# Kernel tuning notes

Measured on AMD Instinct MI355X. Metric: run time of the kernel, lower is better.

## Reference

```python
import jax, jax.numpy as jnp
import numpy as np
import math

HEADS = 16
SPH = 64      # size_per_head
KEY = 64      # key_size (defaults to size_per_head)
EMB = 1024
STEP = 3


def extract_seq_patches(x, kernel_size, step):
    # x: [B, L, D] -> [B, L, kernel_size, D]; patch j at pos t is x_pad[t - p_left + j*step]
    B, L, D = x.shape
    k_size = kernel_size + (step - 1) * (kernel_size - 1)
    p_right = (k_size - 1) // 2
    p_left = k_size - 1 - p_right
    xp = jnp.pad(x, ((0, 0), (p_left, p_right), (0, 0)))
    xs = [xp[:, i:i + L] for i in range(0, k_size, step)]  # kernel_size slices
    return jnp.stack(xs, axis=2)


def setup_inputs() -> dict:
    key = jax.random.key(0)
    kx, kq, kk, kv = jax.random.split(key, 4)
    B, L = 2, 4096
    x = jax.random.normal(kx, (B, L, EMB), dtype=jnp.float32)
    W_q = jax.random.normal(kq, (EMB, HEADS * KEY), dtype=jnp.float32) * 0.02
    W_k = jax.random.normal(kk, (EMB, HEADS * KEY), dtype=jnp.float32) * 0.02
    W_v = jax.random.normal(kv, (EMB, HEADS * SPH), dtype=jnp.float32) * 0.02
    return {"x": x, "W_q": W_q, "W_k": W_k, "W_v": W_v}


def _forward(x, W_q, W_k, W_v):
    B, L, D = x.shape
    pad_len = STEP - L % STEP
    x = jnp.pad(x, ((0, 0), (0, pad_len), (0, 0)))
    new_len = L + pad_len
    blocks = new_len // STEP
    q = x @ W_q  # [B, new_len, H*KEY]
    k = x @ W_k
    v = x @ W_v
    ksz = 1 + 2 * (STEP - 1)  # kernel_size = 5
    kp = extract_seq_patches(k, ksz, STEP)  # [B, new_len, ksz, H*KEY]
    vp = extract_seq_patches(v, ksz, STEP)
    # reshape to [B, H, step, blocks, d]
    q = q.reshape(B, blocks, STEP, HEADS, KEY).transpose(0, 3, 2, 1, 4)
    kb = k.reshape(B, blocks, STEP, HEADS, KEY).transpose(0, 3, 2, 1, 4)
    vb = v.reshape(B, blocks, STEP, HEADS, SPH).transpose(0, 3, 2, 1, 4)
    # neighbor patches: [B, H, step, blocks, ksz, d]
    kp = kp.reshape(B, blocks, STEP, ksz, HEADS, KEY).transpose(0, 4, 2, 1, 3, 5)
    vp = vp.reshape(B, blocks, STEP, ksz, HEADS, SPH).transpose(0, 4, 2, 1, 3, 5)
    scale = 1.0 / math.sqrt(KEY)
    # strided attention over blocks (same residue mod step): [B,H,step,blocks,blocks]
    a = jnp.einsum('bhsqk,bhspk->bhsqp', q, kb) * scale
    # block-local neighbor attention: [B,H,step,blocks,ksz]
    ap = jnp.einsum('bhsqk,bhsqnk->bhsqn', q, kp) * scale
    A = jax.nn.softmax(jnp.concatenate([a, ap], axis=-1), axis=-1)
    a, ap = A[..., :blocks], A[..., blocks:]
    o = (jnp.einsum('bhsqp,bhspd->bhsqd', a, vb)
         + jnp.einsum('bhsqn,bhsqnd->bhsqd', ap, vp))
    o = o.transpose(0, 3, 2, 1, 4).reshape(B, new_len, HEADS * SPH)
    return o[:, :L]


def reference(x, W_q, W_k, W_v):
    return _forward(x, W_q, W_k, W_v)
```

## Files before the change

### kernel.cpp

```cpp
#include <hip/hip_runtime.h>
#include <hip/hip_bf16.h>

typedef unsigned int u32;
typedef unsigned short u16;
typedef short s8v __attribute__((ext_vector_type(8)));
typedef short s4v __attribute__((ext_vector_type(4)));
typedef float f4v __attribute__((ext_vector_type(4)));
typedef float f16v __attribute__((ext_vector_type(16)));
typedef u32 u32x2 __attribute__((ext_vector_type(2)));

#define NBLK 1366
#define VROW 1376
#define QSCALE 0.18033688011112042f

__device__ __forceinline__ u16 f2b(float f) {
  u32 u = __builtin_bit_cast(u32, f);
  u = (u + 0x7FFFu + ((u >> 16) & 1u)) >> 16;
  return (u16)u;
}

__device__ __forceinline__ u32 cvtpk(float a, float b) {
  u32 r;
  asm("v_cvt_pk_bf16_f32 %0, %1, %2" : "=v"(r) : "v"(a), "v"(b));
  return r;
}

__device__ __forceinline__ float fexp2(float x) {
#if defined(__has_builtin)
#if __has_builtin(__builtin_amdgcn_exp2f)
  return __builtin_amdgcn_exp2f(x);
#define FEXP2_DONE 1
#endif
#endif
#ifndef FEXP2_DONE
  float r;
  asm("v_exp_f32 %0, %1" : "=v"(r) : "v"(x));
  return r;
#endif
}

__device__ __forceinline__ void gll16(const void* g, void* l) {
  __builtin_amdgcn_global_load_lds(
      (const __attribute__((address_space(1))) u32*)g,
      (__attribute__((address_space(3))) u32*)l, 16, 0, 0);
}

__device__ __forceinline__ f4v mfma32(s8v a, s8v b, f4v c) {
  return __builtin_amdgcn_mfma_f32_16x16x32_bf16(a, b, c, 0, 0, 0);
}

__device__ __forceinline__ f16v mfma3216(s8v a, s8v b, f16v c) {
  return __builtin_amdgcn_mfma_f32_32x32x16_bf16(a, b, c, 0, 0, 0);
}

__device__ __forceinline__ f16v mfma3208(s4v a, s4v b, f16v c) {
#if defined(__has_builtin)
#if __has_builtin(__builtin_amdgcn_mfma_f32_32x32x8bf16_1k)
#define MFMA3208_BUILTIN 1
#endif
#endif
#ifdef MFMA3208_BUILTIN
  return __builtin_amdgcn_mfma_f32_32x32x8bf16_1k(a, b, c, 0, 0, 0);
#else
  f16v d;
  asm("v_mfma_f32_32x32x8_bf16 %0, %1, %2, %3" : "=v"(d) : "v"(a), "v"(b), "v"(c));
  return d;
#endif
}

__global__ __launch_bounds__(256) void k_prep(const float* __restrict__ x,
                                              const float* __restrict__ Wq,
                                              const float* __restrict__ Wk,
                                              const float* __restrict__ Wv,
                                              u16* __restrict__ xb,
                                              u16* __restrict__ Wt,
                                              u16* __restrict__ Vt) {
  const int bid = blockIdx.x;
  const int tid = threadIdx.x;
  if (bid < 4160) {
    long base = ((long)bid * 256 + tid) * 8;
    if (base >= 8320L * 1024L) return;
    int m = (int)(base >> 10);
    int c = (int)(base & 1023);
    int b = m / 4098;
    int t = m - b * 4098;
    s8v pack;
    if (m < 8196 && t < 4096) {
      const float* src = x + ((size_t)b * 4096 + t) * 1024 + c;
      float4 v0 = *(const float4*)(src);
      float4 v1 = *(const float4*)(src + 4);
      pack[0] = (short)f2b(v0.x); pack[1] = (short)f2b(v0.y);
      pack[2] = (short)f2b(v0.z); pack[3] = (short)f2b(v0.w);
      pack[4] = (short)f2b(v1.x); pack[5] = (short)f2b(v1.y);
      pack[6] = (short)f2b(v1.z); pack[7] = (short)f2b(v1.w);
    } else {
#pragma unroll
      for (int i = 0; i < 8; ++i) pack[i] = 0;
    }
    *(s8v*)(xb + base) = pack;
  } else if (bid < 7232) {
    __shared__ float tile[32][33];
    int bid3 = bid - 4160;
    int z = bid3 >> 10;
    int rem = bid3 & 1023;
    const float* W = (z == 0) ? Wq : ((z == 1) ? Wk : Wv);
    u16* dst = Wt + (size_t)z * 1024 * 1024;
    int n0 = (rem & 31) * 32, k0 = (rem >> 5) * 32;
    int tx = tid & 31, ty = tid >> 5;
#pragma unroll
    for (int i = 0; i < 4; ++i)
      tile[ty + i * 8][tx] = W[(size_t)(k0 + ty + i * 8) * 1024 + n0 + tx];
    __syncthreads();
#pragma unroll
    for (int i = 0; i < 4; ++i)
      dst[(size_t)(n0 + ty + i * 8) * 1024 + k0 + tx] = f2b(tile[tx][ty + i * 8]);
  } else {
    int gidx = (bid - 7232) * 256 + tid;
    if (gidx < 6144) {
      u16* dst = Vt + (size_t)gidx * VROW + NBLK;
#pragma unroll
      for (int i = 0; i < 10; ++i) dst[i] = 0;
    } else if (gidx < 6400) {
      Vt[(size_t)6144 * VROW + (gidx - 6144)] = 0;
    }
  }
}

__global__ __launch_bounds__(256) void k_gemm_qkv(const u16* __restrict__ xb,
                                                  const u16* __restrict__ Wt,
                                                  u16* __restrict__ Qp,
                                                  u16* __restrict__ Kp,
                                                  u16* __restrict__ Vt) {
  const int zid = blockIdx.z;
  const int m0 = blockIdx.x * 128;
  const int n0 = blockIdx.y * 128;
  const u16* Bg = Wt + (size_t)zid * 1024 * 1024 + (size_t)n0 * 1024;

  __shared__ __align__(16) u16 shl[16384];
  u16* A0 = shl;
  u16* A1 = shl + 4096;
  u16* B0 = shl + 8192;
  u16* B1 = shl + 12288;

  const int tid = threadIdx.x;
  const int lane = tid & 63;
  const int w = tid >> 6;
  const int wr = w >> 1, wc = w & 1;
  const int lo = lane & 15, g = lane >> 4;

  const int lrow = lane >> 2;
  const int csrc = (lane & 3) ^ ((lane >> 3) & 3);
  const int rsw = (g ^ ((lo >> 1) & 3)) << 4;

  f4v acc[4][4];
#pragma unroll
  for (int i = 0; i < 4; ++i)
#pragma unroll
    for (int j = 0; j < 4; ++j) {
      f4v z = {0.f, 0.f, 0.f, 0.f};
      acc[i][j] = z;
    }

  auto stage = [&](int kt, u16* Ab, u16* Bb) {
#pragma unroll
    for (int c = 0; c < 2; ++c) {
      int rloc = w * 32 + c * 16 + lrow;
      gll16(xb + (size_t)(m0 + rloc) * 1024 + kt + csrc * 8,
            Ab + (w * 32 + c * 16) * 32);
      gll16(Bg + (size_t)rloc * 1024 + kt + csrc * 8,
            Bb + (w * 32 + c * 16) * 32);
    }
  };

  auto compute = [&](const u16* Ab, const u16* Bb) {
    s8v af[4], bf[4];
#pragma unroll
    for (int i = 0; i < 4; ++i) {
      int ar = wr * 64 + i * 16 + lo;
      af[i] = *(const s8v*)((const char*)Ab + ar * 64 + rsw);
      int br = wc * 64 + i * 16 + lo;
      bf[i] = *(const s8v*)((const char*)Bb + br * 64 + rsw);
    }
    __builtin_amdgcn_s_setprio(1);
#pragma unroll
    for (int i = 0; i < 4; ++i)
#pragma unroll
      for (int j = 0; j < 4; ++j)
        acc[i][j] = mfma32(af[i], bf[j], acc[i][j]);
    __builtin_amdgcn_s_setprio(0);
  };

#define BAR_VM4                                             \
  asm volatile("s_waitcnt vmcnt(4)" ::: "memory");          \
  __builtin_amdgcn_s_barrier();                             \
  asm volatile("" ::: "memory");
#define BAR_LGKM                                            \
  asm volatile("s_waitcnt lgkmcnt(0)" ::: "memory");        \
  __builtin_amdgcn_s_barrier();                             \
  asm volatile("" ::: "memory");

  stage(0, A0, B0);
#pragma unroll 1
  for (int kk = 0; kk < 15; ++kk) {
    int kt = kk * 64;
    stage(kt + 32, A1, B1);
    BAR_VM4
    compute(A0, B0);
    BAR_LGKM
    stage(kt + 64, A0, B0);
    BAR_VM4
    compute(A1, B1);
    BAR_LGKM
  }
  stage(31 * 32, A1, B1);
  BAR_VM4
  compute(A0, B0);
  BAR_LGKM
  asm volatile("s_waitcnt vmcnt(0)" ::: "memory");
  __builtin_amdgcn_s_barrier();
  asm volatile("" ::: "memory");
  compute(A1, B1);
  __syncthreads();

#undef BAR_VM4
#undef BAR_LGKM

  const float esc = (zid == 0) ? QSCALE : 1.0f;
  if (zid != 2) {
    u16* dq = (zid == 0) ? Qp : Kp;
#pragma unroll
    for (int i = 0; i < 4; ++i) {
#pragma unroll
      for (int r = 0; r < 4; ++r) {
        int m = m0 + wr * 64 + i * 16 + g * 4 + r;
        if (m >= 8196) continue;
        int b = m / 4098;
        int t = m - b * 4098;
        int s = t % 3;
        int p = t / 3;
        int cb = (b * 3 + s) * 16;
#pragma unroll
        for (int j = 0; j < 4; ++j) {
          int n = n0 + wc * 64 + j * 16 + lo;
          int h = n >> 6, d = n & 63;
          dq[(size_t)((cb + h) * NBLK + p) * 64 + d] = f2b(acc[i][j][r] * esc);
        }
      }
    }
  } else {
    u16* tile = shl;
#pragma unroll
    for (int i = 0; i < 4; ++i)
#pragma unroll
      for (int r = 0; r < 4; ++r) {
        int ml = wr * 64 + i * 16 + g * 4 + r;
#pragma unroll
        for (int j = 0; j < 4; ++j) {
          int nl = wc * 64 + j * 16 + lo;
          tile[ml * 128 + nl] = f2b(acc[i][j][r]);
        }
      }
    __syncthreads();
    for (int pair = tid; pair < 384; pair += 256) {
      int nl = pair & 127;
      int s = pair >> 7;
      int n = n0 + nl;
      int h = n >> 6, d = n & 63;
      for (int b = 0; b < 2; ++b) {
        int mlo = m0 > b * 4098 ? m0 : b * 4098;
        int cap = b * 4098 + 4096;
        int mhi = (m0 + 128 < cap) ? m0 + 128 : cap;
        if (mlo >= mhi) continue;
        int t_lo = mlo - b * 4098;
        int add = (s - (t_lo % 3) + 3) % 3;
        int t = t_lo + add;
        int tend = mhi - b * 4098;
        u16* dst = Vt + (size_t)(((b * 3 + s) * 16 + h) * 64 + d) * VROW;
        for (; t < tend; t += 3)
          dst[t / 3] = tile[(b * 4098 + t - m0) * 128 + nl];
      }
    }
  }
}

__global__ __launch_bounds__(256, 4) void k_attn(const u16* __restrict__ Qp,
                                                 const u16* __restrict__ Kp,
                                                 const u16* __restrict__ Vt,
                                                 float* __restrict__ out) {
  const int wg = blockIdx.x;
  const int idx = (wg & 7) * 132 + (wg >> 3);
  const int combo = idx / 11;
  const int qb = idx - combo * 11;
  const int b = combo / 48;
  const int rem = combo - b * 48;
  const int s = rem >> 4;
  const int h = rem & 15;
  const int tid = threadIdx.x, lane = tid & 63, w = tid >> 6;
  const int lq = lane & 31, lh = lane >> 5;

  const u16* Qg = Qp + (size_t)combo * (NBLK * 64);
  const u16* Kg = Kp + (size_t)combo * (NBLK * 64);
  const u16* Vg = Vt + (size_t)combo * (64 * VROW);

  __shared__ __align__(16) u16 Kl[64 * 64];
  __shared__ __align__(16) u16 Vl[64 * 64];

  const int qg = qb * 128 + w * 32 + lq;
  const int qc = (qg < NBLK) ? qg : (NBLK - 1);
  s8v qf[4];
#pragma unroll
  for (int ss = 0; ss < 4; ++ss)
    qf[ss] = *(const s8v*)(Qg + (size_t)qc * 64 + ss * 16 + lh * 8);

  s4v onesf;
  onesf[0] = onesf[1] = onesf[2] = onesf[3] = (short)0x3F80;

  f16v oacc0, oacc1, den_acc;
#pragma unroll
  for (int i = 0; i < 16; ++i) { oacc0[i] = 0.f; oacc1[i] = 0.f; den_acc[i] = 0.f; }

  const int srow8 = lane >> 3;
  const int schunk = ((lane & 7) - srow8) & 7;
  const int qmin = qb * 128;

  for (int j0 = 0; j0 < NBLK; j0 += 64) {
    __syncthreads();
#pragma unroll
    for (int c = 0; c < 2; ++c) {
      int rbase = c * 32 + w * 8;
      gll16(Kg + (size_t)(j0 + rbase + srow8) * 64 + schunk * 8, Kl + rbase * 64);
      gll16(Vg + (size_t)(rbase + srow8) * VROW + j0 + schunk * 8, Vl + rbase * 64);
    }
    __syncthreads();

    const bool special = ((j0 <= qmin + 129) && (j0 + 65 >= qmin)) || (j0 + 64 > NBLK);
    s4v ef[8];
#pragma unroll
    for (int jb = 0; jb < 2; ++jb) {
      f16v sacc;
#pragma unroll
      for (int i = 0; i < 16; ++i) sacc[i] = 0.f;
      __builtin_amdgcn_s_setprio(1);
#pragma unroll
      for (int ss = 0; ss < 4; ++ss) {
        s8v kf = *(const s8v*)((const char*)Kl + (jb * 32 + lq) * 128 +
                               ((((ss * 2 + lh) + (lq & 7)) & 7) << 4));
        sacc = mfma3216(kf, qf[ss], sacc);
      }
      __builtin_amdgcn_s_setprio(0);

      if (special) {
        float e[16];
#pragma unroll
        for (int r = 0; r < 16; ++r) {
          int j = j0 + jb * 32 + (r & 3) + 8 * (r >> 2) + 4 * lh;
          float ev = fexp2(sacc[r]);
          int dd = j - qg;
          float fac = (j < NBLK) ? (((dd <= 2) && (dd >= -2)) ? 2.f : 1.f) : 0.f;
          e[r] = ev * fac;
        }
#pragma unroll
        for (int k4 = 0; k4 < 4; ++k4) {
          u32x2 w2;
          w2[0] = cvtpk(e[k4 * 4 + 0], e[k4 * 4 + 1]);
          w2[1] = cvtpk(e[k4 * 4 + 2], e[k4 * 4 + 3]);
          ef[jb * 4 + k4] = __builtin_bit_cast(s4v, w2);
        }
      } else {
#pragma unroll
        for (int k4 = 0; k4 < 4; ++k4) {
          u32x2 w2;
          w2[0] = cvtpk(fexp2(sacc[k4 * 4 + 0]), fexp2(sacc[k4 * 4 + 1]));
          w2[1] = cvtpk(fexp2(sacc[k4 * 4 + 2]), fexp2(sacc[k4 * 4 + 3]));
          ef[jb * 4 + k4] = __builtin_bit_cast(s4v, w2);
        }
      }
    }

    __builtin_amdgcn_s_setprio(1);
#pragma unroll
    for (int ks = 0; ks < 8; ++ks)
      den_acc = mfma3208(ef[ks], onesf, den_acc);
#pragma unroll
    for (int ks = 0; ks < 8; ++ks) {
      const char* vb = (const char*)Vl + lq * 128 +
                       (((ks + (lq & 7)) & 7) << 4) + lh * 8;
      s4v vf0 = *(const s4v*)(vb);
      s4v vf1 = *(const s4v*)(vb + 32 * 128);
      oacc0 = mfma3208(ef[ks], vf0, oacc0);
      oacc1 = mfma3208(ef[ks], vf1, oacc1);
    }
    __builtin_amdgcn_s_setprio(0);
  }

  const int hbase = h * 64;
#pragma unroll
  for (int r = 0; r < 16; ++r) {
    int q = qb * 128 + w * 32 + (r & 3) + 8 * (r >> 2) + 4 * lh;
    float dden = den_acc[r];
    dden += (q == 0 || q == NBLK - 1) ? 2.f : ((q == 1 || q == NBLK - 2) ? 1.f : 0.f);
    float rr = 1.f / dden;
    int t = 3 * q + s;
    if (q < NBLK && t < 4096) {
      float* orow = out + ((size_t)b * 4096 + t) * 1024 + hbase + lq;
      orow[0] = oacc0[r] * rr;
      orow[32] = oacc1[r] * rr;
    }
  }
}

extern "C" void kernel_launch(void* const* d_in, const int* in_sizes, int n_in,
                              void* d_out, int out_size, void* d_ws, size_t ws_size,
                              hipStream_t stream) {
  const float* x  = (const float*)d_in[0];
  const float* Wq = (const float*)d_in[1];
  const float* Wk = (const float*)d_in[2];
  const float* Wv = (const float*)d_in[3];
  float* out = (float*)d_out;

  u16* ws = (u16*)d_ws;
  u16* xb = ws;
  u16* Wt = xb + 8519680;
  u16* Qp = Wt + 3145728;
  u16* Kp = Qp + 8392704;
  u16* Vt = Kp + 8392704;

  k_prep<<<dim3(7257), 256, 0, stream>>>(x, Wq, Wk, Wv, xb, Wt, Vt);
  k_gemm_qkv<<<dim3(65, 8, 3), 256, 0, stream>>>(xb, Wt, Qp, Kp, Vt);
  k_attn<<<dim3(1056), 256, 0, stream>>>(Qp, Kp, Vt, out);
}
```

Measured before the change: 223.2 us.

## Double-buffer K/V tiles via register prefetch with padded LDS layout

Replaces the synchronous global-to-LDS loads with a register-staged double-buffered pipeline. The next tile is loaded into registers while the current one is computed, then written into the alternate LDS slot, leaving one barrier per iteration instead of two. The LDS layout changes from an XOR-swizzled 64x64 tile to padded 36-element rows split into halves, so each lane's K and V fragments are read with simple strided loads. This costs extra registers and LDS space and adds ds_write traffic in exchange for hiding global-load latency. The special-case window bound also changes from qmin+129 to qmin+130.

```diff
diff --git a/kernel.cpp b/kernel.cpp
--- a/kernel.cpp
+++ b/kernel.cpp
@@ -66,6 +66,13 @@
   asm("v_mfma_f32_32x32x8_bf16 %0, %1, %2, %3" : "=v"(d) : "v"(a), "v"(b), "v"(c));
   return d;
 #endif
+}
+
+__device__ __forceinline__ s4v lo4(s8v v) {
+  return __builtin_shufflevector(v, v, 0, 1, 2, 3);
+}
+__device__ __forceinline__ s4v hi4(s8v v) {
+  return __builtin_shufflevector(v, v, 4, 5, 6, 7);
 }
 
 __global__ __launch_bounds__(256) void k_prep(const float* __restrict__ x,
@@ -302,8 +309,7 @@
   const u16* Kg = Kp + (size_t)combo * (NBLK * 64);
   const u16* Vg = Vt + (size_t)combo * (64 * VROW);
 
-  __shared__ __align__(16) u16 Kl[64 * 64];
-  __shared__ __align__(16) u16 Vl[64 * 64];
+  __shared__ __align__(16) u16 att[2][4][64 * 36];
 
   const int qg = qb * 128 + w * 32 + lq;
   const int qc = (qg < NBLK) ? qg : (NBLK - 1);
@@ -319,21 +325,48 @@
 #pragma unroll
   for (int i = 0; i < 16; ++i) { oacc0[i] = 0.f; oacc1[i] = 0.f; den_acc[i] = 0.f; }
 
-  const int srow8 = lane >> 3;
-  const int schunk = ((lane & 7) - srow8) & 7;
+  const int srow = tid >> 2;
+  const int sch = (tid & 3) * 2;
+  const int ssub = (tid & 3) * 8;
+  s8v kr0, kr1, vr0, vr1;
+
+  auto load_regs = [&](int jt) {
+    const int j0 = jt * 64;
+    const u16* kp = Kg + (size_t)(j0 + srow) * 64 + sch * 8;
+    kr0 = *(const s8v*)(kp);
+    kr1 = *(const s8v*)(kp + 8);
+    const u16* vp = Vg + (size_t)srow * VROW + j0 + sch * 8;
+    vr0 = *(const s8v*)(vp);
+    vr1 = *(const s8v*)(vp + 8);
+  };
+
+  auto stage_write = [&](int slot) {
+    u16* K0 = att[slot][0];
+    u16* K1 = att[slot][1];
+    u16* V0 = att[slot][2];
+    u16* V1 = att[slot][3];
+    const int kb = srow * 36 + ssub;
+    *(s4v*)(K0 + kb) = lo4(kr0);
+    *(s4v*)(K0 + kb + 4) = hi4(kr0);
+    *(s4v*)(K1 + kb) = lo4(kr1);
+    *(s4v*)(K1 + kb + 4) = hi4(kr1);
+    const int vb0 = srow * 36 + sch * 4;
+    *(s4v*)(V0 + vb0) = lo4(vr0);
+    *(s4v*)(V1 + vb0) = hi4(vr0);
+    *(s4v*)(V0 + vb0 + 4) = lo4(vr1);
+    *(s4v*)(V1 + vb0 + 4) = hi4(vr1);
+  };
+
   const int qmin = qb * 128;
 
-  for (int j0 = 0; j0 < NBLK; j0 += 64) {
-    __syncthreads();
-#pragma unroll
-    for (int c = 0; c < 2; ++c) {
-      int rbase = c * 32 + w * 8;
-      gll16(Kg + (size_t)(j0 + rbase + srow8) * 64 + schunk * 8, Kl + rbase * 64);
-      gll16(Vg + (size_t)(rbase + srow8) * VROW + j0 + schunk * 8, Vl + rbase * 64);
-    }
-    __syncthreads();
-
-    const bool special = ((j0 <= qmin + 129) && (j0 + 65 >= qmin)) || (j0 + 64 > NBLK);
+  auto compute = [&](int slot, int jt) {
+    const int j0 = jt * 64;
+    const u16* Kb = att[slot][lh];
+    const u16* Vb0 = att[slot][2];
+    const u16* Vb1 = att[slot][3];
+    const u16* Vme = (lh == 0) ? Vb0 : Vb1;
+
+    const bool special = ((j0 <= qmin + 130) && (j0 + 65 >= qmin)) || (j0 + 64 > NBLK);
     s4v ef[8];
 #pragma unroll
     for (int jb = 0; jb < 2; ++jb) {
@@ -343,8 +376,10 @@
       __builtin_amdgcn_s_setprio(1);
 #pragma unroll
       for (int ss = 0; ss < 4; ++ss) {
-        s8v kf = *(const s8v*)((const char*)Kl + (jb * 32 + lq) * 128 +
-                               ((((ss * 2 + lh) + (lq & 7)) & 7) << 4));
+        const u16* kp = Kb + (jb * 32 + lq) * 36 + ss * 8;
+        s4v a = *(const s4v*)kp;
+        s4v b2 = *(const s4v*)(kp + 4);
+        s8v kf = __builtin_shufflevector(a, b2, 0, 1, 2, 3, 4, 5, 6, 7);
         sacc = mfma3216(kf, qf[ss], sacc);
       }
       __builtin_amdgcn_s_setprio(0);
@@ -383,15 +418,34 @@
       den_acc = mfma3208(ef[ks], onesf, den_acc);
 #pragma unroll
     for (int ks = 0; ks < 8; ++ks) {
-      const char* vb = (const char*)Vl + lq * 128 +
-                       (((ks + (lq & 7)) & 7) << 4) + lh * 8;
-      s4v vf0 = *(const s4v*)(vb);
-      s4v vf1 = *(const s4v*)(vb + 32 * 128);
+      s4v vf0 = *(const s4v*)(Vme + lq * 36 + ks * 4);
+      s4v vf1 = *(const s4v*)(Vme + (32 + lq) * 36 + ks * 4);
       oacc0 = mfma3208(ef[ks], vf0, oacc0);
       oacc1 = mfma3208(ef[ks], vf1, oacc1);
     }
     __builtin_amdgcn_s_setprio(0);
+  };
+
+#define LGKM_BAR                                            \
+  asm volatile("s_waitcnt lgkmcnt(0)" ::: "memory");        \
+  __builtin_amdgcn_s_barrier();                             \
+  asm volatile("" ::: "memory");
+
+  load_regs(0);
+  stage_write(0);
+  load_regs(1);
+  LGKM_BAR
+
+#pragma unroll 1
+  for (int t = 0; t < 21; ++t) {
+    compute(t & 1, t);
+    stage_write((t + 1) & 1);
+    if (t < 20) load_regs(t + 2);
+    LGKM_BAR
   }
+  compute(1, 21);
+
+#undef LGKM_BAR
 
   const int hbase = h * 64;
 #pragma unroll
```

Result: faster. 217.6 us (-2.5%).
